# Optimization experiments

Hardware: AMD Instinct MI355X
Metric: run time of the kernel (lower is better)

The kernel has to match this reference:

```python
import jax, jax.numpy as jnp
import numpy as np

NEG_SLOPE = 0.2


def _gat_conv(x, src, dst, W, a_src, a_dst, b, n_nodes):
    # Single-head PyG GATConv (normalize arg in source is ignored by GATConv).
    h = x @ W                                   # [N, C_out]
    e_src = h @ a_src                           # [N] alpha_src contribution
    e_dst = h @ a_dst                           # [N] alpha_dst contribution
    logits = jax.nn.leaky_relu(e_src[src] + e_dst[dst], NEG_SLOPE)  # [E]
    m = jax.ops.segment_max(logits, dst, num_segments=n_nodes)      # per-dst max
    e = jnp.exp(logits - m[dst])
    denom = jax.ops.segment_sum(e, dst, num_segments=n_nodes)
    alpha = e / denom[dst]                      # edge softmax over in-neighbors
    out = jax.ops.segment_sum(h[src] * alpha[:, None], dst, num_segments=n_nodes)
    return out + b


def _add_self_loops(edge_index, n_nodes):
    loop = jnp.arange(n_nodes, dtype=edge_index.dtype)
    src = jnp.concatenate([edge_index[0], loop])
    dst = jnp.concatenate([edge_index[1], loop])
    return src, dst


def setup_inputs() -> dict:
    key = jax.random.key(0)
    ks = jax.random.split(key, 16)
    N, E, C_IN, C_HID, C_OUT = 50000, 1600000, 128, 128, 64
    x = jax.random.normal(ks[0], (N, C_IN), dtype=jnp.float32)
    edge_index = jax.random.randint(ks[1], (2, E), 0, N, dtype=jnp.int32)
    glorot = lambda k, shape: jax.random.normal(k, shape, jnp.float32) * np.sqrt(2.0 / sum(shape))
    return {
        "x": x,
        "edge_index": edge_index,
        "W0": glorot(ks[2], (C_IN, C_HID)),
        "as0": glorot(ks[3], (C_HID,)) * 0.1,
        "ad0": glorot(ks[4], (C_HID,)) * 0.1,
        "b0": jnp.zeros((C_HID,), jnp.float32),
        "W1": glorot(ks[5], (C_HID, C_HID)),
        "as1": glorot(ks[6], (C_HID,)) * 0.1,
        "ad1": glorot(ks[7], (C_HID,)) * 0.1,
        "b1": jnp.zeros((C_HID,), jnp.float32),
        "W2": glorot(ks[8], (C_HID, C_OUT)),
        "as2": glorot(ks[9], (C_OUT,)) * 0.1,
        "ad2": glorot(ks[10], (C_OUT,)) * 0.1,
        "b2": jnp.zeros((C_OUT,), jnp.float32),
    }


def reference(x, edge_index, W0, as0, ad0, b0, W1, as1, ad1, b1, W2, as2, ad2, b2):
    n_nodes = x.shape[0]
    src, dst = _add_self_loops(edge_index, n_nodes)
    # eval mode: F.dropout with training=False is identity
    h = jax.nn.relu(_gat_conv(x, src, dst, W0, as0, ad0, b0, n_nodes))
    h = jax.nn.relu(_gat_conv(h, src, dst, W1, as1, ad1, b1, n_nodes))
    out = _gat_conv(h, src, dst, W2, as2, ad2, b2, n_nodes)
    return out
```

## Files before the change

kernel.cpp:

```cpp
#include <hip/hip_runtime.h>
#include <hip/hip_bf16.h>
#include <type_traits>

#define DEVFN __device__ __forceinline__

typedef __attribute__((ext_vector_type(8))) short bfrag;
typedef __attribute__((ext_vector_type(4))) float facc4;
typedef __attribute__((ext_vector_type(2))) float f32x2;

DEVFN float lrelu(float v) { return (v >= 0.f) ? v : 0.2f * v; }

DEVFN float bf_lo(unsigned u) { return __uint_as_float(u << 16); }
DEVFN float bf_hi(unsigned u) { return __uint_as_float(u & 0xFFFF0000u); }
DEVFN f32x2 upk2(unsigned u) {
  f32x2 r; r.x = bf_lo(u); r.y = bf_hi(u); return r;
}
DEVFN unsigned short f2bf(float f) {
  __hip_bfloat16 h = __float2bfloat16(f);
  return *reinterpret_cast<unsigned short*>(&h);
}
DEVFN unsigned packbf2(float x, float y) {
  return (unsigned)f2bf(x) | ((unsigned)f2bf(y) << 16);
}

DEVFN float wave_sum(float v) {
#pragma unroll
  for (int o = 1; o < 64; o <<= 1) v += __shfl_xor(v, o, 64);
  return v;
}
DEVFN float wave_max(float v) {
#pragma unroll
  for (int o = 1; o < 64; o <<= 1) v = fmaxf(v, __shfl_xor(v, o, 64));
  return v;
}

#define FMA_ROW(p_, v_)                                                  \
  {                                                                      \
    f32x2 pv; pv.x = (p_); pv.y = (p_);                                  \
    acc2[0] += pv * upk2((v_).x);                                        \
    acc2[1] += pv * upk2((v_).y);                                        \
    acc2[2] += pv * upk2((v_).z);                                        \
    acc2[3] += pv * upk2((v_).w);                                        \
  }

template<int C, bool A_FP32>
__global__ __launch_bounds__(256) void gemm_mfma(const void* __restrict__ Xin,
                                                 const float* __restrict__ W,
                                                 const float* __restrict__ a_src,
                                                 const float* __restrict__ a_dst,
                                                 unsigned short* __restrict__ H,
                                                 float* __restrict__ es,
                                                 float* __restrict__ ed,
                                                 int N) {
  constexpr int K = 128;
  constexpr int LSTR = K + 8;
  constexpr int NT = C / 16;
  __shared__ unsigned short WsT[C * LSTR];

  const int t = threadIdx.x;
  for (int i = t; i < K * C; i += 256) {
    int k = i / C;
    int c = i - k * C;
    WsT[c * LSTR + k] = f2bf(W[i]);
  }
  __syncthreads();

  const int wave = t >> 6;
  const int lane = t & 63;
  const int l15 = lane & 15;
  const int quad = lane >> 4;
  const int arow = blockIdx.x * 64 + wave * 16 + l15;
  const bool avalid = arow < N;

  facc4 acc[NT];
#pragma unroll
  for (int i = 0; i < NT; ++i) acc[i] = (facc4){0.f, 0.f, 0.f, 0.f};

#pragma unroll
  for (int ks = 0; ks < 4; ++ks) {
    bfrag a;
    if (A_FP32) {
      if (avalid) {
        const float* xp = (const float*)Xin + (size_t)arow * K + quad * 8 + ks * 32;
        float4 u = *(const float4*)xp;
        float4 v = *(const float4*)(xp + 4);
        a[0] = (short)f2bf(u.x); a[1] = (short)f2bf(u.y);
        a[2] = (short)f2bf(u.z); a[3] = (short)f2bf(u.w);
        a[4] = (short)f2bf(v.x); a[5] = (short)f2bf(v.y);
        a[6] = (short)f2bf(v.z); a[7] = (short)f2bf(v.w);
      } else {
        a = (bfrag){0, 0, 0, 0, 0, 0, 0, 0};
      }
    } else {
      const unsigned short* xp =
          (const unsigned short*)Xin + (size_t)arow * K + quad * 8 + ks * 32;
      a = *(const bfrag*)xp;
    }
#pragma unroll
    for (int ct = 0; ct < NT; ++ct) {
      bfrag b = *(const bfrag*)(&WsT[(ct * 16 + l15) * LSTR + ks * 32 + quad * 8]);
      acc[ct] = __builtin_amdgcn_mfma_f32_16x16x32_bf16(a, b, acc[ct], 0, 0, 0);
    }
  }

  float asv[NT], adv[NT];
#pragma unroll
  for (int ct = 0; ct < NT; ++ct) {
    asv[ct] = a_src[ct * 16 + l15];
    adv[ct] = a_dst[ct * 16 + l15];
  }

  const int orow0 = blockIdx.x * 64 + wave * 16 + quad * 4;
#pragma unroll
  for (int r = 0; r < 4; ++r) {
    const int orow = orow0 + r;
    float ps = 0.f, pd = 0.f;
#pragma unroll
    for (int ct = 0; ct < NT; ++ct) {
      if (orow < N) H[(size_t)orow * C + ct * 16 + l15] = f2bf(acc[ct][r]);
      ps += acc[ct][r] * asv[ct];
      pd += acc[ct][r] * adv[ct];
    }
#pragma unroll
    for (int msk = 1; msk < 16; msk <<= 1) {
      ps += __shfl_xor(ps, msk, 64);
      pd += __shfl_xor(pd, msk, 64);
    }
    if (l15 == 0 && orow < N) { es[orow] = ps; ed[orow] = pd; }
  }
}

__global__ void hist_only(const int* __restrict__ dst, int* __restrict__ hmat,
                          int E, int nbk, int chunk) {
  __shared__ int hist[4 * 128];
  const int t = threadIdx.x;
  for (int i = t; i < 4 * 128; i += 256) hist[i] = 0;
  __syncthreads();
  int* h = &hist[(t >> 6) << 7];
  const int e0 = blockIdx.x * chunk;
  const int e1 = min(E, e0 + chunk);
  for (int e = e0 + t; e < e1; e += 256) {
    atomicAdd(&h[dst[e] >> 9], 1);
  }
  __syncthreads();
  if (t < nbk)
    hmat[t * gridDim.x + blockIdx.x] =
        hist[t] + hist[t + 128] + hist[t + 256] + hist[t + 384];
}

__global__ void scan_partial(const int* __restrict__ in, int* __restrict__ csum, int n) {
  __shared__ int sh[256];
  int i = blockIdx.x * 256 + threadIdx.x;
  sh[threadIdx.x] = (i < n) ? in[i] : 0;
  __syncthreads();
  for (int o = 128; o > 0; o >>= 1) {
    if (threadIdx.x < o) sh[threadIdx.x] += sh[threadIdx.x + o];
    __syncthreads();
  }
  if (threadIdx.x == 0) csum[blockIdx.x] = sh[0];
}

__global__ void scan_chunks(int* __restrict__ csum, int nch) {
  __shared__ int sh[256];
  __shared__ int carry;
  if (threadIdx.x == 0) carry = 0;
  __syncthreads();
  for (int base = 0; base < nch; base += 256) {
    int i = base + threadIdx.x;
    int v = (i < nch) ? csum[i] : 0;
    sh[threadIdx.x] = v;
    __syncthreads();
    for (int o = 1; o < 256; o <<= 1) {
      int t = (threadIdx.x >= o) ? sh[threadIdx.x - o] : 0;
      __syncthreads();
      sh[threadIdx.x] += t;
      __syncthreads();
    }
    if (i < nch) csum[i] = carry + sh[threadIdx.x] - v;
    __syncthreads();
    if (threadIdx.x == 255) carry += sh[255];
    __syncthreads();
  }
}

__global__ void scan_final(const int* __restrict__ deg, const int* __restrict__ csum,
                           int* __restrict__ rp, int* __restrict__ wp, int N, int E) {
  __shared__ int sh[256];
  int i = blockIdx.x * 256 + threadIdx.x;
  int v = (i < N) ? deg[i] : 0;
  sh[threadIdx.x] = v;
  __syncthreads();
  for (int o = 1; o < 256; o <<= 1) {
    int t = (threadIdx.x >= o) ? sh[threadIdx.x - o] : 0;
    __syncthreads();
    sh[threadIdx.x] += t;
    __syncthreads();
  }
  if (i < N) {
    int r = csum[blockIdx.x] + sh[threadIdx.x] - v;
    rp[i] = r;
    wp[i] = r;
  }
  if (blockIdx.x == 0 && threadIdx.x == 0) rp[N] = E;
}

__global__ void scan_final_excl(const int* __restrict__ in, const int* __restrict__ csum,
                                int* __restrict__ out, int n) {
  __shared__ int sh[256];
  int i = blockIdx.x * 256 + threadIdx.x;
  int v = (i < n) ? in[i] : 0;
  sh[threadIdx.x] = v;
  __syncthreads();
  for (int o = 1; o < 256; o <<= 1) {
    int t = (threadIdx.x >= o) ? sh[threadIdx.x - o] : 0;
    __syncthreads();
    sh[threadIdx.x] += t;
    __syncthreads();
  }
  if (i < n) out[i] = csum[blockIdx.x] + sh[threadIdx.x] - v;
}

__global__ void place_pass(const int* __restrict__ src, const int* __restrict__ dst,
                           const int* __restrict__ off, int2* __restrict__ be,
                           int E, int nbk, int chunk) {
  __shared__ int cur[128];
  const int t = threadIdx.x;
  if (t < nbk) cur[t] = off[t * gridDim.x + blockIdx.x];
  __syncthreads();
  const int e0 = blockIdx.x * chunk;
  const int e1 = min(E, e0 + chunk);
  for (int e = e0 + t; e < e1; e += 256) {
    int d = dst[e];
    int s = src[e];
    int p = atomicAdd(&cur[d >> 9], 1);
    be[p] = make_int2(s, d);
  }
}

__global__ void bucket_final(const int2* __restrict__ be, const int* __restrict__ off,
                             int* __restrict__ rp, unsigned short* __restrict__ col,
                             int E, int N, int nbk, int pblk) {
  __shared__ int cur[512];
  __shared__ int ps[256];
  const int b = blockIdx.x;
  const int n0 = b << 9;
  const int cnt = min(512, N - n0);
  const int t = threadIdx.x;
  for (int i = t; i < cnt; i += 256) cur[i] = 0;
  __syncthreads();
  const int e0 = off[b * pblk];
  const int e1 = (b + 1 < nbk) ? off[(b + 1) * pblk] : E;
  for (int e = e0 + t; e < e1; e += 256) {
    int2 sd = be[e];
    atomicAdd(&cur[sd.y - n0], 1);
  }
  __syncthreads();
  const int i0 = 2 * t, i1 = 2 * t + 1;
  const int v0 = (i0 < cnt) ? cur[i0] : 0;
  const int v1 = (i1 < cnt) ? cur[i1] : 0;
  ps[t] = v0 + v1;
  __syncthreads();
  for (int o = 1; o < 256; o <<= 1) {
    int u = (t >= o) ? ps[t - o] : 0;
    __syncthreads();
    ps[t] += u;
    __syncthreads();
  }
  const int base = e0 + ps[t] - (v0 + v1);
  if (i0 < cnt) { rp[n0 + i0] = base;      cur[i0] = base; }
  if (i1 < cnt) { rp[n0 + i1] = base + v0; cur[i1] = base + v0; }
  if (b == nbk - 1 && t == 0) rp[N] = E;
  __syncthreads();
  for (int e = e0 + t; e < e1; e += 256) {
    int2 sd = be[e];
    int p = atomicAdd(&cur[sd.y - n0], 1);
    col[p] = (unsigned short)sd.x;
  }
}

__global__ void csr_scatter_ranged(const int* __restrict__ src,
                                   const int* __restrict__ dst,
                                   int* __restrict__ wp, int* __restrict__ col,
                                   int E, int range, int npass) {
  const int stride = gridDim.x * blockDim.x;
  const int gid = blockIdx.x * blockDim.x + threadIdx.x;
  for (int pass = 0; pass < npass; ++pass) {
    const int lo = pass * range;
    const int hi = lo + range;
    for (int e = gid; e < E; e += stride) {
      int d = dst[e];
      if (d >= lo && d < hi) {
        int p = atomicAdd(wp + d, 1);
        col[p] = src[e];
      }
    }
  }
}

__global__ void csr_count(const int* __restrict__ dst, int* __restrict__ deg, int E) {
  int e = blockIdx.x * blockDim.x + threadIdx.x;
  if (e < E) atomicAdd(deg + dst[e], 1);
}

template<typename IT>
__global__ void gat_alpha(const int* __restrict__ row_ptr,
                          const IT* __restrict__ col,
                          const float* __restrict__ es,
                          const float* __restrict__ ed,
                          float* __restrict__ P,
                          float* __restrict__ DENI,
                          float* __restrict__ SPV, int N) {
  const int lane = threadIdx.x & 63;
  const int n = blockIdx.x * (blockDim.x >> 6) + (threadIdx.x >> 6);
  if (n >= N) return;

  const int k0 = row_ptr[n];
  const int k1 = row_ptr[n + 1];
  const int deg = k1 - k0;
  const float edd = ed[n];
  const float self_lg = lrelu(es[n] + edd);

  if (deg <= 64) {
    int k = k0 + lane;
    bool act = (k < k1);
    int c = act ? (int)col[k] : 0;
    float lg = act ? lrelu(es[c] + edd) : -3.0e38f;
    float m = fmaxf(wave_max(lg), self_lg);
    float p = act ? __expf(lg - m) : 0.f;
    float sp = __expf(self_lg - m);
    float den = wave_sum(p) + sp;
    if (act) P[k] = p;
    if (lane == 0) { DENI[n] = 1.f / den; SPV[n] = sp; }
  } else {
    float mloc = self_lg;
    for (int base = k0; base < k1; base += 64) {
      int k = base + lane;
      if (k < k1) mloc = fmaxf(mloc, lrelu(es[(int)col[k]] + edd));
    }
    float m = wave_max(mloc);
    float sp = __expf(self_lg - m);
    float den = sp;
    for (int base = k0; base < k1; base += 64) {
      int k = base + lane;
      bool act = (k < k1);
      float p = act ? __expf(lrelu(es[(int)col[k]] + edd) - m) : 0.f;
      den += wave_sum(p);
      if (act) P[k] = p;
    }
    if (lane == 0) { DENI[n] = 1.f / den; SPV[n] = sp; }
  }
}

template<bool RELU, typename IT>
__global__ void gat_gather128(const int* __restrict__ row_ptr,
                              const IT* __restrict__ col,
                              const float* __restrict__ P,
                              const float* __restrict__ DENI,
                              const float* __restrict__ SPV,
                              const unsigned short* __restrict__ H,
                              const float* __restrict__ bias,
                              void* __restrict__ outX, int N) {
  const int lane = threadIdx.x & 63;
  const int n = blockIdx.x * (blockDim.x >> 6) + (threadIdx.x >> 6);
  if (n >= N) return;

  const int g4 = lane >> 4;
  const int l15 = lane & 15;

  const int k0 = row_ptr[n];
  const int k1 = row_ptr[n + 1];
  const int deg = k1 - k0;
  const float sp = SPV[n];
  const float inv = DENI[n];

  const char* Hb = (const char*)H;
  f32x2 acc2[4];
#pragma unroll
  for (int i = 0; i < 4; ++i) { acc2[i].x = 0.f; acc2[i].y = 0.f; }

  if (deg <= 64) {
    int k = k0 + lane;
    bool act = (k < k1);
    int c = act ? (int)col[k] : 0;
    float p = act ? P[k] : 0.f;
#pragma unroll 2
    for (int j = 0; j < deg; j += 8) {
      int i0 = min(j + g4, 63);
      int i1 = min(j + 4 + g4, 63);
      int c0 = __shfl(c, i0);
      int c1 = __shfl(c, i1);
      float p0 = __shfl(p, i0);
      float p1 = __shfl(p, i1);
      uint4 v0 = *(const uint4*)(Hb + (((size_t)c0 << 8) + l15 * 16));
      uint4 v1 = *(const uint4*)(Hb + (((size_t)c1 << 8) + l15 * 16));
      FMA_ROW(p0, v0);
      FMA_ROW(p1, v1);
    }
  } else {
    for (int base = k0; base < k1; base += 64) {
      int k = base + lane;
      bool act = (k < k1);
      int c = act ? (int)col[k] : 0;
      float p = act ? P[k] : 0.f;
      int len = min(64, k1 - base);
#pragma unroll 2
      for (int j = 0; j < len; j += 8) {
        int i0 = min(j + g4, 63);
        int i1 = min(j + 4 + g4, 63);
        int c0 = __shfl(c, i0);
        int c1 = __shfl(c, i1);
        float p0 = __shfl(p, i0);
        float p1 = __shfl(p, i1);
        uint4 v0 = *(const uint4*)(Hb + (((size_t)c0 << 8) + l15 * 16));
        uint4 v1 = *(const uint4*)(Hb + (((size_t)c1 << 8) + l15 * 16));
        FMA_ROW(p0, v0);
        FMA_ROW(p1, v1);
      }
    }
  }

  float a[8];
#pragma unroll
  for (int i = 0; i < 4; ++i) { a[2 * i] = acc2[i].x; a[2 * i + 1] = acc2[i].y; }
#pragma unroll
  for (int i = 0; i < 8; ++i) {
    a[i] += __shfl_xor(a[i], 16, 64);
    a[i] += __shfl_xor(a[i], 32, 64);
  }

  uint4 hv = *(const uint4*)(Hb + (((size_t)n << 8) + l15 * 16));
  a[0] += sp * bf_lo(hv.x); a[1] += sp * bf_hi(hv.x);
  a[2] += sp * bf_lo(hv.y); a[3] += sp * bf_hi(hv.y);
  a[4] += sp * bf_lo(hv.z); a[5] += sp * bf_hi(hv.z);
  a[6] += sp * bf_lo(hv.w); a[7] += sp * bf_hi(hv.w);

  float4 bv0 = *(const float4*)(bias + l15 * 8);
  float4 bv1 = *(const float4*)(bias + l15 * 8 + 4);
  float o0 = a[0] * inv + bv0.x, o1 = a[1] * inv + bv0.y;
  float o2 = a[2] * inv + bv0.z, o3 = a[3] * inv + bv0.w;
  float o4 = a[4] * inv + bv1.x, o5 = a[5] * inv + bv1.y;
  float o6 = a[6] * inv + bv1.z, o7 = a[7] * inv + bv1.w;
  if (RELU) {
    o0 = fmaxf(o0, 0.f); o1 = fmaxf(o1, 0.f); o2 = fmaxf(o2, 0.f);
    o3 = fmaxf(o3, 0.f); o4 = fmaxf(o4, 0.f); o5 = fmaxf(o5, 0.f);
    o6 = fmaxf(o6, 0.f); o7 = fmaxf(o7, 0.f);
  }
  if (g4 == 0) {
    uint4 w;
    w.x = packbf2(o0, o1); w.y = packbf2(o2, o3);
    w.z = packbf2(o4, o5); w.w = packbf2(o6, o7);
    *(uint4*)((char*)outX + (((size_t)n << 8) + l15 * 16)) = w;
  }
}

template<bool RELU, typename IT>
__global__ void gat_gather64(const int* __restrict__ row_ptr,
                             const IT* __restrict__ col,
                             const float* __restrict__ P,
                             const float* __restrict__ DENI,
                             const float* __restrict__ SPV,
                             const unsigned short* __restrict__ H,
                             const float* __restrict__ bias,
                             float* __restrict__ outX, int N) {
  const int lane = threadIdx.x & 63;
  const int n = blockIdx.x * (blockDim.x >> 6) + (threadIdx.x >> 6);
  if (n >= N) return;

  const int g8 = lane >> 3;
  const int l8 = lane & 7;

  const int k0 = row_ptr[n];
  const int k1 = row_ptr[n + 1];
  const int deg = k1 - k0;
  const float sp = SPV[n];
  const float inv = DENI[n];

  const char* Hb = (const char*)H;
  f32x2 acc2[4];
#pragma unroll
  for (int i = 0; i < 4; ++i) { acc2[i].x = 0.f; acc2[i].y = 0.f; }

  if (deg <= 64) {
    int k = k0 + lane;
    bool act = (k < k1);
    int c = act ? (int)col[k] : 0;
    float p = act ? P[k] : 0.f;
#pragma unroll 2
    for (int j = 0; j < deg; j += 8) {
      int i0 = min(j + g8, 63);
      int c0 = __shfl(c, i0);
      float p0 = __shfl(p, i0);
      uint4 v0 = *(const uint4*)(Hb + (((size_t)c0 << 7) + l8 * 16));
      FMA_ROW(p0, v0);
    }
  } else {
    for (int base = k0; base < k1; base += 64) {
      int k = base + lane;
      bool act = (k < k1);
      int c = act ? (int)col[k] : 0;
      float p = act ? P[k] : 0.f;
      int len = min(64, k1 - base);
#pragma unroll 2
      for (int j = 0; j < len; j += 8) {
        int i0 = min(j + g8, 63);
        int c0 = __shfl(c, i0);
        float p0 = __shfl(p, i0);
        uint4 v0 = *(const uint4*)(Hb + (((size_t)c0 << 7) + l8 * 16));
        FMA_ROW(p0, v0);
      }
    }
  }

  float a[8];
#pragma unroll
  for (int i = 0; i < 4; ++i) { a[2 * i] = acc2[i].x; a[2 * i + 1] = acc2[i].y; }
#pragma unroll
  for (int i = 0; i < 8; ++i) {
    a[i] += __shfl_xor(a[i], 8, 64);
    a[i] += __shfl_xor(a[i], 16, 64);
    a[i] += __shfl_xor(a[i], 32, 64);
  }

  uint4 hv = *(const uint4*)(Hb + (((size_t)n << 7) + l8 * 16));
  a[0] += sp * bf_lo(hv.x); a[1] += sp * bf_hi(hv.x);
  a[2] += sp * bf_lo(hv.y); a[3] += sp * bf_hi(hv.y);
  a[4] += sp * bf_lo(hv.z); a[5] += sp * bf_hi(hv.z);
  a[6] += sp * bf_lo(hv.w); a[7] += sp * bf_hi(hv.w);

  float4 bv0 = *(const float4*)(bias + l8 * 8);
  float4 bv1 = *(const float4*)(bias + l8 * 8 + 4);
  float4 w0, w1;
  w0.x = a[0] * inv + bv0.x; w0.y = a[1] * inv + bv0.y;
  w0.z = a[2] * inv + bv0.z; w0.w = a[3] * inv + bv0.w;
  w1.x = a[4] * inv + bv1.x; w1.y = a[5] * inv + bv1.y;
  w1.z = a[6] * inv + bv1.z; w1.w = a[7] * inv + bv1.w;
  if (RELU) {
    w0.x = fmaxf(w0.x, 0.f); w0.y = fmaxf(w0.y, 0.f);
    w0.z = fmaxf(w0.z, 0.f); w0.w = fmaxf(w0.w, 0.f);
    w1.x = fmaxf(w1.x, 0.f); w1.y = fmaxf(w1.y, 0.f);
    w1.z = fmaxf(w1.z, 0.f); w1.w = fmaxf(w1.w, 0.f);
  }
  if (g8 == 0) {
    char* op = (char*)outX + (((size_t)n << 8) + l8 * 32);
    *(float4*)op = w0;
    *(float4*)(op + 16) = w1;
  }
}


extern "C" void kernel_launch(void* const* d_in, const int* in_sizes, int n_in,
                              void* d_out, int out_size, void* d_ws, size_t ws_size,
                              hipStream_t stream) {
  const int C_HID = in_sizes[3];
  const int C_FIN = in_sizes[11];
  const int C_IN  = in_sizes[2] / C_HID;
  const int N     = in_sizes[0] / C_IN;
  const int E     = in_sizes[1] / 2;
  const int NPAD  = ((N + 63) / 64) * 64;

  const float* x = (const float*)d_in[0];
  const int* ei  = (const int*)d_in[1];
  const int* src = ei;
  const int* dst = ei + E;

  const float* W0  = (const float*)d_in[2];
  const float* as0 = (const float*)d_in[3];
  const float* ad0 = (const float*)d_in[4];
  const float* b0  = (const float*)d_in[5];
  const float* W1  = (const float*)d_in[6];
  const float* as1 = (const float*)d_in[7];
  const float* ad1 = (const float*)d_in[8];
  const float* b1  = (const float*)d_in[9];
  const float* W2  = (const float*)d_in[10];
  const float* as2 = (const float*)d_in[11];
  const float* ad2 = (const float*)d_in[12];
  const float* b2  = (const float*)d_in[13];

  char* base = (char*)d_ws;
  size_t off = 0;
  auto alloc = [&](size_t bytes) -> char* {
    char* p = base + off;
    off = (off + bytes + 255) & ~((size_t)255);
    return p;
  };
  const int PBLK = 512;
  const int NBK  = (N + 511) >> 9;
  const int M    = NBK * PBLK;
  const int NCH  = (N + 255) / 256;
  const int MCH  = (M + 255) / 256;
  const int SCH  = (NCH > MCH ? NCH : MCH);

  unsigned short* XB  = (unsigned short*)alloc((size_t)NPAD * C_HID * 2);
  unsigned short* H   = (unsigned short*)alloc((size_t)N * C_HID * 2);
  float* ES    = (float*)alloc((size_t)N * sizeof(float));
  float* ED    = (float*)alloc((size_t)N * sizeof(float));
  float* P     = (float*)alloc((size_t)E * sizeof(float));
  float* DENI  = (float*)alloc((size_t)N * sizeof(float));
  float* SPV   = (float*)alloc((size_t)N * sizeof(float));
  int*   RP    = (int*)alloc((size_t)(N + 1) * sizeof(int));
  int*   WP    = (int*)alloc((size_t)N * sizeof(int));
  void*  COL   = (void*)alloc((size_t)E * sizeof(int));
  int*   DEG   = (int*)alloc((size_t)N * sizeof(int));
  int*   CSUM  = (int*)alloc((size_t)SCH * sizeof(int));
  int*   HMAT  = (int*)alloc((size_t)M * sizeof(int));
  int*   OFF   = (int*)alloc((size_t)M * sizeof(int));
  int2*  BE    = (int2*)alloc((size_t)E * sizeof(int2));
  (void)ws_size;

  const int wgrid = (N + 3) / 4;
  const int mgrid = NPAD / 64;
  const bool u16 = (N <= 65535);

  if (u16) {
    const int CHUNK = (E + PBLK - 1) / PBLK;
    hist_only<<<PBLK, 256, 0, stream>>>(dst, HMAT, E, NBK, CHUNK);
    scan_partial<<<MCH, 256, 0, stream>>>(HMAT, CSUM, M);
    scan_chunks<<<1, 256, 0, stream>>>(CSUM, MCH);
    scan_final_excl<<<MCH, 256, 0, stream>>>(HMAT, CSUM, OFF, M);
    place_pass<<<PBLK, 256, 0, stream>>>(src, dst, OFF, BE, E, NBK, CHUNK);
    bucket_final<<<NBK, 256, 0, stream>>>(BE, OFF, RP, (unsigned short*)COL,
                                          E, N, NBK, PBLK);
  } else {
    hipMemsetAsync(DEG, 0, (size_t)N * sizeof(int), stream);
    const int ET256 = (E + 255) / 256;
    csr_count<<<ET256, 256, 0, stream>>>(dst, DEG, E);
    scan_partial<<<NCH, 256, 0, stream>>>(DEG, CSUM, N);
    scan_chunks<<<1, 256, 0, stream>>>(CSUM, NCH);
    scan_final<<<NCH, 256, 0, stream>>>(DEG, CSUM, RP, WP, N, E);
    const int NPASS = 8;
    const int range = (N + NPASS - 1) / NPASS;
    csr_scatter_ranged<<<2048, 256, 0, stream>>>(src, dst, WP, (int*)COL, E,
                                                 range, NPASS);
  }

  auto run_layers = [&](auto* col) {
    using IT = typename std::remove_pointer<decltype(col)>::type;
    gemm_mfma<128, true><<<mgrid, 256, 0, stream>>>(x, W0, as0, ad0, H, ES, ED, N);
    gat_alpha<IT><<<wgrid, 256, 0, stream>>>(RP, col, ES, ED, P, DENI, SPV, N);
    gat_gather128<true, IT><<<wgrid, 256, 0, stream>>>(RP, col, P, DENI, SPV,
                                                       H, b0, XB, N);
    gemm_mfma<128, false><<<mgrid, 256, 0, stream>>>(XB, W1, as1, ad1, H, ES, ED, N);
    gat_alpha<IT><<<wgrid, 256, 0, stream>>>(RP, col, ES, ED, P, DENI, SPV, N);
    gat_gather128<true, IT><<<wgrid, 256, 0, stream>>>(RP, col, P, DENI, SPV,
                                                       H, b1, XB, N);
    gemm_mfma<64, false><<<mgrid, 256, 0, stream>>>(XB, W2, as2, ad2, H, ES, ED, N);
    gat_alpha<IT><<<wgrid, 256, 0, stream>>>(RP, col, ES, ED, P, DENI, SPV, N);
    gat_gather64<false, IT><<<wgrid, 256, 0, stream>>>(RP, col, P, DENI, SPV,
                                                       H, b2, (float*)d_out, N);
  };

  if (u16) run_layers((unsigned short*)COL);
  else     run_layers((int*)COL);
  (void)out_size; (void)n_in;
}
```

Before: 369.5 us.

## Fuse edge softmax into gather kernels and pack bucketed edges into 32 bits

Merges the per-layer alpha kernel into the gather kernel, so edge softmax weights are computed in registers and never stored to or reloaded from a per-edge P buffer. This also removes the DENI/SPV arrays and three launches. The gather loop now software-pipelines the H row loads, issuing the next batch before the FMAs on the current one. Bucketed (src,dst) pairs are packed as two 16-bit halves in one 32-bit word instead of int2, halving that traffic. The packing relies on N fitting in 16 bits, which the u16 path already assumes.

```diff
diff --git a/kernel.cpp b/kernel.cpp
--- a/kernel.cpp
+++ b/kernel.cpp
@@ -221,7 +221,7 @@
 }
 
 __global__ void place_pass(const int* __restrict__ src, const int* __restrict__ dst,
-                           const int* __restrict__ off, int2* __restrict__ be,
+                           const int* __restrict__ off, unsigned* __restrict__ be,
                            int E, int nbk, int chunk) {
   __shared__ int cur[128];
   const int t = threadIdx.x;
@@ -233,11 +233,11 @@
     int d = dst[e];
     int s = src[e];
     int p = atomicAdd(&cur[d >> 9], 1);
-    be[p] = make_int2(s, d);
-  }
-}
-
-__global__ void bucket_final(const int2* __restrict__ be, const int* __restrict__ off,
+    be[p] = (unsigned)s | ((unsigned)d << 16);
+  }
+}
+
+__global__ void bucket_final(const unsigned* __restrict__ be, const int* __restrict__ off,
                              int* __restrict__ rp, unsigned short* __restrict__ col,
                              int E, int N, int nbk, int pblk) {
   __shared__ int cur[512];
@@ -251,8 +251,8 @@
   const int e0 = off[b * pblk];
   const int e1 = (b + 1 < nbk) ? off[(b + 1) * pblk] : E;
   for (int e = e0 + t; e < e1; e += 256) {
-    int2 sd = be[e];
-    atomicAdd(&cur[sd.y - n0], 1);
+    unsigned sd = be[e];
+    atomicAdd(&cur[(int)(sd >> 16) - n0], 1);
   }
   __syncthreads();
   const int i0 = 2 * t, i1 = 2 * t + 1;
@@ -272,9 +272,9 @@
   if (b == nbk - 1 && t == 0) rp[N] = E;
   __syncthreads();
   for (int e = e0 + t; e < e1; e += 256) {
-    int2 sd = be[e];
-    int p = atomicAdd(&cur[sd.y - n0], 1);
-    col[p] = (unsigned short)sd.x;
+    unsigned sd = be[e];
+    int p = atomicAdd(&cur[(int)(sd >> 16) - n0], 1);
+    col[p] = (unsigned short)(sd & 0xFFFFu);
   }
 }
 
@@ -302,23 +302,32 @@
   if (e < E) atomicAdd(deg + dst[e], 1);
 }
 
-template<typename IT>
-__global__ void gat_alpha(const int* __restrict__ row_ptr,
-                          const IT* __restrict__ col,
-                          const float* __restrict__ es,
-                          const float* __restrict__ ed,
-                          float* __restrict__ P,
-                          float* __restrict__ DENI,
-                          float* __restrict__ SPV, int N) {
+template<bool RELU, typename IT>
+__global__ void gat_fused128(const int* __restrict__ row_ptr,
+                             const IT* __restrict__ col,
+                             const float* __restrict__ es,
+                             const float* __restrict__ ed,
+                             const unsigned short* __restrict__ H,
+                             const float* __restrict__ bias,
+                             void* __restrict__ outX, int N) {
   const int lane = threadIdx.x & 63;
   const int n = blockIdx.x * (blockDim.x >> 6) + (threadIdx.x >> 6);
   if (n >= N) return;
+
+  const int g4 = lane >> 4;
+  const int l15 = lane & 15;
 
   const int k0 = row_ptr[n];
   const int k1 = row_ptr[n + 1];
   const int deg = k1 - k0;
   const float edd = ed[n];
   const float self_lg = lrelu(es[n] + edd);
+
+  const char* Hb = (const char*)H;
+  f32x2 acc2[4];
+#pragma unroll
+  for (int i = 0; i < 4; ++i) { acc2[i].x = 0.f; acc2[i].y = 0.f; }
+  float den, sp;
 
   if (deg <= 64) {
     int k = k0 + lane;
@@ -327,10 +336,35 @@
     float lg = act ? lrelu(es[c] + edd) : -3.0e38f;
     float m = fmaxf(wave_max(lg), self_lg);
     float p = act ? __expf(lg - m) : 0.f;
-    float sp = __expf(self_lg - m);
-    float den = wave_sum(p) + sp;
-    if (act) P[k] = p;
-    if (lane == 0) { DENI[n] = 1.f / den; SPV[n] = sp; }
+    sp = __expf(self_lg - m);
+    den = wave_sum(p) + sp;
+
+    if (deg > 0) {
+      int i0 = g4;
+      int i1 = min(4 + g4, 63);
+      int c0 = __shfl(c, i0);
+      int c1 = __shfl(c, i1);
+      uint4 v0 = *(const uint4*)(Hb + (((size_t)c0 << 8) + l15 * 16));
+      uint4 v1 = *(const uint4*)(Hb + (((size_t)c1 << 8) + l15 * 16));
+      const int nb = (deg + 7) >> 3;
+      for (int t = 0; t + 1 < nb; ++t) {
+        int ni0 = min(8 * t + 8 + g4, 63);
+        int ni1 = min(8 * t + 12 + g4, 63);
+        int nc0 = __shfl(c, ni0);
+        int nc1 = __shfl(c, ni1);
+        uint4 u0 = *(const uint4*)(Hb + (((size_t)nc0 << 8) + l15 * 16));
+        uint4 u1 = *(const uint4*)(Hb + (((size_t)nc1 << 8) + l15 * 16));
+        float p0 = __shfl(p, i0);
+        float p1 = __shfl(p, i1);
+        FMA_ROW(p0, v0);
+        FMA_ROW(p1, v1);
+        v0 = u0; v1 = u1; i0 = ni0; i1 = ni1;
+      }
+      float p0 = __shfl(p, i0);
+      float p1 = __shfl(p, i1);
+      FMA_ROW(p0, v0);
+      FMA_ROW(p1, v1);
+    }
   } else {
     float mloc = self_lg;
     for (int base = k0; base < k1; base += 64) {
@@ -338,72 +372,15 @@
       if (k < k1) mloc = fmaxf(mloc, lrelu(es[(int)col[k]] + edd));
     }
     float m = wave_max(mloc);
-    float sp = __expf(self_lg - m);
-    float den = sp;
-    for (int base = k0; base < k1; base += 64) {
-      int k = base + lane;
-      bool act = (k < k1);
-      float p = act ? __expf(lrelu(es[(int)col[k]] + edd) - m) : 0.f;
-      den += wave_sum(p);
-      if (act) P[k] = p;
-    }
-    if (lane == 0) { DENI[n] = 1.f / den; SPV[n] = sp; }
-  }
-}
-
-template<bool RELU, typename IT>
-__global__ void gat_gather128(const int* __restrict__ row_ptr,
-                              const IT* __restrict__ col,
-                              const float* __restrict__ P,
-                              const float* __restrict__ DENI,
-                              const float* __restrict__ SPV,
-                              const unsigned short* __restrict__ H,
-                              const float* __restrict__ bias,
-                              void* __restrict__ outX, int N) {
-  const int lane = threadIdx.x & 63;
-  const int n = blockIdx.x * (blockDim.x >> 6) + (threadIdx.x >> 6);
-  if (n >= N) return;
-
-  const int g4 = lane >> 4;
-  const int l15 = lane & 15;
-
-  const int k0 = row_ptr[n];
-  const int k1 = row_ptr[n + 1];
-  const int deg = k1 - k0;
-  const float sp = SPV[n];
-  const float inv = DENI[n];
-
-  const char* Hb = (const char*)H;
-  f32x2 acc2[4];
-#pragma unroll
-  for (int i = 0; i < 4; ++i) { acc2[i].x = 0.f; acc2[i].y = 0.f; }
-
-  if (deg <= 64) {
-    int k = k0 + lane;
-    bool act = (k < k1);
-    int c = act ? (int)col[k] : 0;
-    float p = act ? P[k] : 0.f;
-#pragma unroll 2
-    for (int j = 0; j < deg; j += 8) {
-      int i0 = min(j + g4, 63);
-      int i1 = min(j + 4 + g4, 63);
-      int c0 = __shfl(c, i0);
-      int c1 = __shfl(c, i1);
-      float p0 = __shfl(p, i0);
-      float p1 = __shfl(p, i1);
-      uint4 v0 = *(const uint4*)(Hb + (((size_t)c0 << 8) + l15 * 16));
-      uint4 v1 = *(const uint4*)(Hb + (((size_t)c1 << 8) + l15 * 16));
-      FMA_ROW(p0, v0);
-      FMA_ROW(p1, v1);
-    }
-  } else {
+    sp = __expf(self_lg - m);
+    den = sp;
     for (int base = k0; base < k1; base += 64) {
       int k = base + lane;
       bool act = (k < k1);
       int c = act ? (int)col[k] : 0;
-      float p = act ? P[k] : 0.f;
+      float p = act ? __expf(lrelu(es[c] + edd) - m) : 0.f;
+      den += wave_sum(p);
       int len = min(64, k1 - base);
-#pragma unroll 2
       for (int j = 0; j < len; j += 8) {
         int i0 = min(j + g4, 63);
         int i1 = min(j + 4 + g4, 63);
@@ -434,6 +411,7 @@
   a[4] += sp * bf_lo(hv.z); a[5] += sp * bf_hi(hv.z);
   a[6] += sp * bf_lo(hv.w); a[7] += sp * bf_hi(hv.w);
 
+  float inv = 1.f / den;
   float4 bv0 = *(const float4*)(bias + l15 * 8);
   float4 bv1 = *(const float4*)(bias + l15 * 8 + 4);
   float o0 = a[0] * inv + bv0.x, o1 = a[1] * inv + bv0.y;
@@ -454,14 +432,13 @@
 }
 
 template<bool RELU, typename IT>
-__global__ void gat_gather64(const int* __restrict__ row_ptr,
-                             const IT* __restrict__ col,
-                             const float* __restrict__ P,
-                             const float* __restrict__ DENI,
-                             const float* __restrict__ SPV,
-                             const unsigned short* __restrict__ H,
-                             const float* __restrict__ bias,
-                             float* __restrict__ outX, int N) {
+__global__ void gat_fused64(const int* __restrict__ row_ptr,
+                            const IT* __restrict__ col,
+                            const float* __restrict__ es,
+                            const float* __restrict__ ed,
+                            const unsigned short* __restrict__ H,
+                            const float* __restrict__ bias,
+                            float* __restrict__ outX, int N) {
   const int lane = threadIdx.x & 63;
   const int n = blockIdx.x * (blockDim.x >> 6) + (threadIdx.x >> 6);
   if (n >= N) return;
@@ -472,35 +449,64 @@
   const int k0 = row_ptr[n];
   const int k1 = row_ptr[n + 1];
   const int deg = k1 - k0;
-  const float sp = SPV[n];
-  const float inv = DENI[n];
+  const float edd = ed[n];
+  const float self_lg = lrelu(es[n] + edd);
 
   const char* Hb = (const char*)H;
   f32x2 acc2[4];
 #pragma unroll
   for (int i = 0; i < 4; ++i) { acc2[i].x = 0.f; acc2[i].y = 0.f; }
+  float den, sp;
 
   if (deg <= 64) {
     int k = k0 + lane;
     bool act = (k < k1);
     int c = act ? (int)col[k] : 0;
-    float p = act ? P[k] : 0.f;
-#pragma unroll 2
-    for (int j = 0; j < deg; j += 8) {
-      int i0 = min(j + g8, 63);
+    float lg = act ? lrelu(es[c] + edd) : -3.0e38f;
+    float m = fmaxf(wave_max(lg), self_lg);
+    float p = act ? __expf(lg - m) : 0.f;
+    sp = __expf(self_lg - m);
+    den = wave_sum(p) + sp;
+
+    if (deg > 0) {
+      int i0 = min(g8, 63);
+      int i1 = min(8 + g8, 63);
       int c0 = __shfl(c, i0);
+      int c1 = __shfl(c, i1);
+      uint4 v0 = *(const uint4*)(Hb + (((size_t)c0 << 7) + l8 * 16));
+      uint4 v1 = *(const uint4*)(Hb + (((size_t)c1 << 7) + l8 * 16));
+      const int nb = (deg + 7) >> 3;
+      for (int t = 0; t + 2 < nb; ++t) {
+        int ni = min(8 * t + 16 + g8, 63);
+        int nc = __shfl(c, ni);
+        uint4 u = *(const uint4*)(Hb + (((size_t)nc << 7) + l8 * 16));
+        float p0 = __shfl(p, i0);
+        FMA_ROW(p0, v0);
+        v0 = v1; v1 = u; i0 = i1; i1 = ni;
+      }
       float p0 = __shfl(p, i0);
-      uint4 v0 = *(const uint4*)(Hb + (((size_t)c0 << 7) + l8 * 16));
       FMA_ROW(p0, v0);
+      if (nb > 1) {
+        float p1 = __shfl(p, i1);
+        FMA_ROW(p1, v1);
+      }
     }
   } else {
+    float mloc = self_lg;
+    for (int base = k0; base < k1; base += 64) {
+      int k = base + lane;
+      if (k < k1) mloc = fmaxf(mloc, lrelu(es[(int)col[k]] + edd));
+    }
+    float m = wave_max(mloc);
+    sp = __expf(self_lg - m);
+    den = sp;
     for (int base = k0; base < k1; base += 64) {
       int k = base + lane;
       bool act = (k < k1);
       int c = act ? (int)col[k] : 0;
-      float p = act ? P[k] : 0.f;
+      float p = act ? __expf(lrelu(es[c] + edd) - m) : 0.f;
+      den += wave_sum(p);
       int len = min(64, k1 - base);
-#pragma unroll 2
       for (int j = 0; j < len; j += 8) {
         int i0 = min(j + g8, 63);
         int c0 = __shfl(c, i0);
@@ -527,6 +533,7 @@
   a[4] += sp * bf_lo(hv.z); a[5] += sp * bf_hi(hv.z);
   a[6] += sp * bf_lo(hv.w); a[7] += sp * bf_hi(hv.w);
 
+  float inv = 1.f / den;
   float4 bv0 = *(const float4*)(bias + l8 * 8);
   float4 bv1 = *(const float4*)(bias + l8 * 8 + 4);
   float4 w0, w1;
@@ -594,9 +601,6 @@
   unsigned short* H   = (unsigned short*)alloc((size_t)N * C_HID * 2);
   float* ES    = (float*)alloc((size_t)N * sizeof(float));
   float* ED    = (float*)alloc((size_t)N * sizeof(float));
-  float* P     = (float*)alloc((size_t)E * sizeof(float));
-  float* DENI  = (float*)alloc((size_t)N * sizeof(float));
-  float* SPV   = (float*)alloc((size_t)N * sizeof(float));
   int*   RP    = (int*)alloc((size_t)(N + 1) * sizeof(int));
   int*   WP    = (int*)alloc((size_t)N * sizeof(int));
   void*  COL   = (void*)alloc((size_t)E * sizeof(int));
@@ -604,7 +608,7 @@
   int*   CSUM  = (int*)alloc((size_t)SCH * sizeof(int));
   int*   HMAT  = (int*)alloc((size_t)M * sizeof(int));
   int*   OFF   = (int*)alloc((size_t)M * sizeof(int));
-  int2*  BE    = (int2*)alloc((size_t)E * sizeof(int2));
+  unsigned* BE = (unsigned*)alloc((size_t)E * sizeof(unsigned));
   (void)ws_size;
 
   const int wgrid = (N + 3) / 4;
@@ -636,17 +640,12 @@
   auto run_layers = [&](auto* col) {
     using IT = typename std::remove_pointer<decltype(col)>::type;
     gemm_mfma<128, true><<<mgrid, 256, 0, stream>>>(x, W0, as0, ad0, H, ES, ED, N);
-    gat_alpha<IT><<<wgrid, 256, 0, stream>>>(RP, col, ES, ED, P, DENI, SPV, N);
-    gat_gather128<true, IT><<<wgrid, 256, 0, stream>>>(RP, col, P, DENI, SPV,
-                                                       H, b0, XB, N);
+    gat_fused128<true, IT><<<wgrid, 256, 0, stream>>>(RP, col, ES, ED, H, b0, XB, N);
     gemm_mfma<128, false><<<mgrid, 256, 0, stream>>>(XB, W1, as1, ad1, H, ES, ED, N);
-    gat_alpha<IT><<<wgrid, 256, 0, stream>>>(RP, col, ES, ED, P, DENI, SPV, N);
-    gat_gather128<true, IT><<<wgrid, 256, 0, stream>>>(RP, col, P, DENI, SPV,
-                                                       H, b1, XB, N);
+    gat_fused128<true, IT><<<wgrid, 256, 0, stream>>>(RP, col, ES, ED, H, b1, XB, N);
     gemm_mfma<64, false><<<mgrid, 256, 0, stream>>>(XB, W2, as2, ad2, H, ES, ED, N);
-    gat_alpha<IT><<<wgrid, 256, 0, stream>>>(RP, col, ES, ED, P, DENI, SPV, N);
-    gat_gather64<false, IT><<<wgrid, 256, 0, stream>>>(RP, col, P, DENI, SPV,
-                                                       H, b2, (float*)d_out, N);
+    gat_fused64<false, IT><<<wgrid, 256, 0, stream>>>(RP, col, ES, ED, H, b2,
+                                                      (float*)d_out, N);
   };
 
   if (u16) run_layers((unsigned short*)COL);
```

New measurement: 334.8 us. 9.4% less time.
